# Optimization experiments

Measured on AMD Instinct MI355X. Metric: run time of the kernel, lower is better.

## Reference

```python
import jax, jax.numpy as jnp
import numpy as np

PAD = 4  # matches init pad


def setup_inputs() -> dict:
    key = jax.random.key(0)
    k1, k2 = jax.random.split(key)
    n, t, c, h, w = 256, 4, 3, 96, 96
    # raw pixel values in [0, 255) like uint8 frames, stored as float32
    img = jax.random.uniform(k1, (n, t, c, h, w), dtype=jnp.float32) * 255.0
    # integer shift per batch element, same across time: randint(0, 2*pad+1, (n, 2))
    shift = jax.random.randint(k2, (n, 2), 0, 2 * PAD + 1, dtype=jnp.int32)
    return {"img": img, "shift": shift}


def reference(img, shift):
    """ShiftImgPreprocessor.forward (train path, eval=False).

    Original: normalize, replicate-pad by PAD, then bilinear grid_sample with a
    grid of pixel-center coords offset by an integer shift (in units of
    2/(h+2*pad)). Because the shift is an exact integer number of pixels and the
    base grid hits pixel centers exactly (align_corners=False), the bilinear
    sample is an exact integer gather: out[b,t,c,i,j] = padded[b,t,c,i+sy, j+sx].
    All sampled coords stay inside the padded image, so padding_mode='zeros'
    never triggers.
    """
    n, t, c, h, w = img.shape
    x = img / 255.0 - 0.5
    # replicate pad H and W by PAD
    xp = jnp.pad(x, ((0, 0), (0, 0), (0, 0), (PAD, PAD), (PAD, PAD)), mode="edge")

    def shift_one(xp_b, s):
        # s[0] is the x (width) shift, s[1] is the y (height) shift
        return jax.lax.dynamic_slice(xp_b, (0, 0, s[1], s[0]), (t, c, h, w))

    return jax.vmap(shift_one)(xp, shift)
```

## Files before the change

### kernel.cpp

```cpp
#include <hip/hip_runtime.h>


#define PAD 4
#define NB  256
#define TT  4
#define CC  3
#define HH  96
#define WW  96
#define W4  (WW / 4)
#define ROWS_PER_B (TT * CC * HH)
#define V4_PER_B (ROWS_PER_B * W4)
#define BLOCK 256

typedef float vfloat4 __attribute__((ext_vector_type(4)));

__global__ __launch_bounds__(BLOCK) void ShiftImgPreprocessor_36679020708143_kernel(
    const float* __restrict__ img,
    const int*   __restrict__ shift,
    float*       __restrict__ out)
{
    const int b = blockIdx.y;
    const int v = blockIdx.x * BLOCK + threadIdx.x;

    const int j4 = v % W4;
    const int r_ = v / W4;
    const int i  = r_ % HH;
    const int tc = r_ / HH;

    const int dx = shift[2 * b + 0] - PAD;
    const int dy = shift[2 * b + 1] - PAD;

    const int yy = min(max(i + dy, 0), HH - 1);

    const size_t plane = ((size_t)b * (TT * CC) + tc) * (size_t)(HH * WW);
    const float* __restrict__ srcrow = img + plane + (size_t)yy * WW;

    const int j = j4 * 4;
    const float k = 1.0f / 255.0f;
    vfloat4 o;

    if (j4 == 0 || j4 == W4 - 1) {
        const int x0 = min(max(j + 0 + dx, 0), WW - 1);
        const int x1 = min(max(j + 1 + dx, 0), WW - 1);
        const int x2 = min(max(j + 2 + dx, 0), WW - 1);
        const int x3 = min(max(j + 3 + dx, 0), WW - 1);
        o = (vfloat4){srcrow[x0], srcrow[x1], srcrow[x2], srcrow[x3]};
    } else {
        const int s  = j + dx;
        const int a4 = s >> 2;
        const int r  = dx & 3;
        const vfloat4* __restrict__ sv = (const vfloat4*)srcrow;
        const vfloat4 V0 = sv[a4];
        const vfloat4 V1 = sv[min(a4 + 1, W4 - 1)];
        switch (r) {
            case 0:  o = V0; break;
            case 1:  o = (vfloat4){V0.y, V0.z, V0.w, V1.x}; break;
            case 2:  o = (vfloat4){V0.z, V0.w, V1.x, V1.y}; break;
            default: o = (vfloat4){V0.w, V1.x, V1.y, V1.z}; break;
        }
    }

    o = o * k - 0.5f;

    vfloat4* outv = (vfloat4*)(out + plane + (size_t)i * WW + j);
    *outv = o;
}

extern "C" void kernel_launch(void* const* d_in, const int* in_sizes, int n_in,
                              void* d_out, int out_size, void* d_ws, size_t ws_size,
                              hipStream_t stream) {
    const float* img   = (const float*)d_in[0];
    const int*   shift = (const int*)d_in[1];
    float*       out   = (float*)d_out;

    dim3 grid(V4_PER_B / BLOCK, NB);
    ShiftImgPreprocessor_36679020708143_kernel<<<grid, BLOCK, 0, stream>>>(img, shift, out);
}
```

Measured before the change: 194.0 us.

## Use persistent grid-stride blocks with software-pipelined load of next tile

```diff
diff --git a/kernel.cpp b/kernel.cpp
--- a/kernel.cpp
+++ b/kernel.cpp
@@ -8,62 +8,99 @@
 #define HH  96
 #define WW  96
 #define W4  (WW / 4)
-#define ROWS_PER_B (TT * CC * HH)
-#define V4_PER_B (ROWS_PER_B * W4)
+#define TC  (TT * CC)
+#define HW  (HH * WW)
+#define V4B (TC * HH * W4)
 #define BLOCK 256
+#define TPB (V4B / BLOCK)
+#define TILES (NB * TPB)
+#define NBLK 2048
 
 typedef float vfloat4 __attribute__((ext_vector_type(4)));
 
-__global__ __launch_bounds__(BLOCK) void ShiftImgPreprocessor_36679020708143_kernel(
+__device__ __forceinline__ void stage_load(
+    int tile, int tid,
+    const float* __restrict__ img, const int* __restrict__ shift,
+    float* __restrict__ out,
+    vfloat4* A, vfloat4* B, int* s_, int* dx_, float** dst)
+{
+    const int b    = tile / TPB;
+    const int tloc = tile - b * TPB;
+    const int vb   = tloc * BLOCK + tid;
+    const int j4   = vb % W4;
+    const int r_   = vb / W4;
+    const int i    = r_ % HH;
+    const int tc   = r_ / HH;
+
+    const int dx = shift[2 * b + 0] - PAD;
+    const int dy = shift[2 * b + 1] - PAD;
+    const int yy = min(max(i + dy, 0), HH - 1);
+
+    const size_t plane = ((size_t)b * TC + tc) * HW;
+    const vfloat4* __restrict__ sv = (const vfloat4*)(img + plane + (size_t)yy * WW);
+
+    const int j  = j4 * 4;
+    const int s  = j + dx;
+    const int a4 = s >> 2;
+    const int a0 = min(max(a4, 0), W4 - 1);
+    const int a1 = min(a4 + 1, W4 - 1);
+
+    *A = sv[a0];
+    *B = sv[a1];
+    *s_  = s;
+    *dx_ = dx;
+    *dst = out + plane + (size_t)i * WW + j;
+}
+
+__device__ __forceinline__ void consume_store(
+    vfloat4 A, vfloat4 B, int s, int dx, float* __restrict__ dst)
+{
+    vfloat4 o;
+    switch (dx & 3) {
+        case 0:  o = A; break;
+        case 1:  o = (vfloat4){A.y, A.z, A.w, B.x}; break;
+        case 2:  o = (vfloat4){A.z, A.w, B.x, B.y}; break;
+        default: o = (vfloat4){A.w, B.x, B.y, B.z}; break;
+    }
+    if (s < 0 || s > WW - 4) {
+        switch (dx) {
+            case -4: o = (vfloat4){A.x, A.x, A.x, A.x}; break;
+            case -3: o = (vfloat4){A.x, A.x, A.x, A.x}; break;
+            case -2: o = (vfloat4){A.x, A.x, A.x, A.y}; break;
+            case -1: o = (vfloat4){A.x, A.x, A.y, A.z}; break;
+            case  1: o = (vfloat4){A.y, A.z, A.w, A.w}; break;
+            case  2: o = (vfloat4){A.z, A.w, A.w, A.w}; break;
+            default: o = (vfloat4){A.w, A.w, A.w, A.w}; break;
+        }
+    }
+    o = o * (1.0f / 255.0f) - 0.5f;
+    *(vfloat4*)dst = o;
+}
+
+__global__ __launch_bounds__(BLOCK, 8) void ShiftImgPreprocessor_36679020708143_kernel(
     const float* __restrict__ img,
     const int*   __restrict__ shift,
     float*       __restrict__ out)
 {
-    const int b = blockIdx.y;
-    const int v = blockIdx.x * BLOCK + threadIdx.x;
+    const int tid = threadIdx.x;
+    int tile = blockIdx.x;
 
-    const int j4 = v % W4;
-    const int r_ = v / W4;
-    const int i  = r_ % HH;
-    const int tc = r_ / HH;
+    vfloat4 A0, B0; int s0, dx0; float* d0;
+    stage_load(tile, tid, img, shift, out, &A0, &B0, &s0, &dx0, &d0);
 
-    const int dx = shift[2 * b + 0] - PAD;
-    const int dy = shift[2 * b + 1] - PAD;
-
-    const int yy = min(max(i + dy, 0), HH - 1);
-
-    const size_t plane = ((size_t)b * (TT * CC) + tc) * (size_t)(HH * WW);
-    const float* __restrict__ srcrow = img + plane + (size_t)yy * WW;
-
-    const int j = j4 * 4;
-    const float k = 1.0f / 255.0f;
-    vfloat4 o;
-
-    if (j4 == 0 || j4 == W4 - 1) {
-        const int x0 = min(max(j + 0 + dx, 0), WW - 1);
-        const int x1 = min(max(j + 1 + dx, 0), WW - 1);
-        const int x2 = min(max(j + 2 + dx, 0), WW - 1);
-        const int x3 = min(max(j + 3 + dx, 0), WW - 1);
-        o = (vfloat4){srcrow[x0], srcrow[x1], srcrow[x2], srcrow[x3]};
-    } else {
-        const int s  = j + dx;
-        const int a4 = s >> 2;
-        const int r  = dx & 3;
-        const vfloat4* __restrict__ sv = (const vfloat4*)srcrow;
-        const vfloat4 V0 = sv[a4];
-        const vfloat4 V1 = sv[min(a4 + 1, W4 - 1)];
-        switch (r) {
-            case 0:  o = V0; break;
-            case 1:  o = (vfloat4){V0.y, V0.z, V0.w, V1.x}; break;
-            case 2:  o = (vfloat4){V0.z, V0.w, V1.x, V1.y}; break;
-            default: o = (vfloat4){V0.w, V1.x, V1.y, V1.z}; break;
+    for (;;) {
+        const int nt = tile + NBLK;
+        if (nt < TILES) {
+            vfloat4 A1, B1; int s1, dx1; float* d1;
+            stage_load(nt, tid, img, shift, out, &A1, &B1, &s1, &dx1, &d1);
+            consume_store(A0, B0, s0, dx0, d0);
+            A0 = A1; B0 = B1; s0 = s1; dx0 = dx1; d0 = d1;
+            tile = nt;
+        } else {
+            consume_store(A0, B0, s0, dx0, d0);
+            break;
         }
     }
-
-    o = o * k - 0.5f;
-
-    vfloat4* outv = (vfloat4*)(out + plane + (size_t)i * WW + j);
-    *outv = o;
 }
 
 extern "C" void kernel_launch(void* const* d_in, const int* in_sizes, int n_in,
@@ -73,6 +110,5 @@
     const int*   shift = (const int*)d_in[1];
     float*       out   = (float*)d_out;
 
-    dim3 grid(V4_PER_B / BLOCK, NB);
-    ShiftImgPreprocessor_36679020708143_kernel<<<grid, BLOCK, 0, stream>>>(img, shift, out);
+    ShiftImgPreprocessor_36679020708143_kernel<<<dim3(NBLK), BLOCK, 0, stream>>>(img, shift, out);
 }
```

After: 198.2 us. 1.02x slower.

## Stage row tiles in LDS with replicated halo for shifted copy

Applied to the files above, without the earlier changes.

```diff
diff --git a/kernel.cpp b/kernel.cpp
--- a/kernel.cpp
+++ b/kernel.cpp
@@ -8,9 +8,15 @@
 #define HH  96
 #define WW  96
 #define W4  (WW / 4)
-#define ROWS_PER_B (TT * CC * HH)
-#define V4_PER_B (ROWS_PER_B * W4)
-#define BLOCK 256
+#define TC  (TT * CC)
+#define HW  (HH * WW)
+#define RPB 16
+#define BPP (HH / RPB)
+#define BLOCK 128
+#define F4PB (RPB * W4)
+#define PERT (F4PB / BLOCK)
+#define LROW 104
+#define NBLK (NB * TC * BPP)
 
 typedef float vfloat4 __attribute__((ext_vector_type(4)));
 
@@ -19,51 +25,55 @@
     const int*   __restrict__ shift,
     float*       __restrict__ out)
 {
-    const int b = blockIdx.y;
-    const int v = blockIdx.x * BLOCK + threadIdx.x;
+    __shared__ float lds[RPB][LROW];
 
-    const int j4 = v % W4;
-    const int r_ = v / W4;
-    const int i  = r_ % HH;
-    const int tc = r_ / HH;
+    const int blk = blockIdx.x;
+    const int bp  = blk / BPP;
+    const int rb  = blk - bp * BPP;
+    const int b   = bp / TC;
+    const int i0  = rb * RPB;
+    const int t   = threadIdx.x;
 
     const int dx = shift[2 * b + 0] - PAD;
     const int dy = shift[2 * b + 1] - PAD;
 
-    const int yy = min(max(i + dy, 0), HH - 1);
+    const size_t plane = (size_t)bp * HW;
+    const float* __restrict__ src = img + plane;
+    float*       __restrict__ dst = out + plane;
 
-    const size_t plane = ((size_t)b * (TT * CC) + tc) * (size_t)(HH * WW);
-    const float* __restrict__ srcrow = img + plane + (size_t)yy * WW;
+    #pragma unroll
+    for (int p = 0; p < PERT; ++p) {
+        const int u = t + p * BLOCK;
+        const int k = u / W4;
+        const int c = u - k * W4;
+        const int yy = min(max(i0 + k + dy, 0), HH - 1);
+        const vfloat4 v = *(const vfloat4*)(src + (size_t)yy * WW + 4 * c);
+        *(vfloat4*)&lds[k][4 + 4 * c] = v;
+    }
+    __syncthreads();
 
-    const int j = j4 * 4;
-    const float k = 1.0f / 255.0f;
-    vfloat4 o;
+    if (t < RPB) {
+        const float e = lds[t][4];
+        lds[t][0] = e; lds[t][1] = e; lds[t][2] = e; lds[t][3] = e;
+    } else if (t < 2 * RPB) {
+        const int k = t - RPB;
+        const float e = lds[k][99];
+        lds[k][100] = e; lds[k][101] = e; lds[k][102] = e; lds[k][103] = e;
+    }
+    __syncthreads();
 
-    if (j4 == 0 || j4 == W4 - 1) {
-        const int x0 = min(max(j + 0 + dx, 0), WW - 1);
-        const int x1 = min(max(j + 1 + dx, 0), WW - 1);
-        const int x2 = min(max(j + 2 + dx, 0), WW - 1);
-        const int x3 = min(max(j + 3 + dx, 0), WW - 1);
-        o = (vfloat4){srcrow[x0], srcrow[x1], srcrow[x2], srcrow[x3]};
-    } else {
-        const int s  = j + dx;
-        const int a4 = s >> 2;
-        const int r  = dx & 3;
-        const vfloat4* __restrict__ sv = (const vfloat4*)srcrow;
-        const vfloat4 V0 = sv[a4];
-        const vfloat4 V1 = sv[min(a4 + 1, W4 - 1)];
-        switch (r) {
-            case 0:  o = V0; break;
-            case 1:  o = (vfloat4){V0.y, V0.z, V0.w, V1.x}; break;
-            case 2:  o = (vfloat4){V0.z, V0.w, V1.x, V1.y}; break;
-            default: o = (vfloat4){V0.w, V1.x, V1.y, V1.z}; break;
-        }
+    const float kk = 1.0f / 255.0f;
+    #pragma unroll
+    for (int p = 0; p < PERT; ++p) {
+        const int u = t + p * BLOCK;
+        const int k = u / W4;
+        const int c = u - k * W4;
+        const float* lp = &lds[k][0] + (4 + 4 * c + dx);
+        vfloat4 v;
+        __builtin_memcpy(&v, lp, sizeof(v));
+        v = v * kk - 0.5f;
+        *(vfloat4*)(dst + (size_t)(i0 + k) * WW + 4 * c) = v;
     }
-
-    o = o * k - 0.5f;
-
-    vfloat4* outv = (vfloat4*)(out + plane + (size_t)i * WW + j);
-    *outv = o;
 }
 
 extern "C" void kernel_launch(void* const* d_in, const int* in_sizes, int n_in,
@@ -73,6 +83,5 @@
     const int*   shift = (const int*)d_in[1];
     float*       out   = (float*)d_out;
 
-    dim3 grid(V4_PER_B / BLOCK, NB);
-    ShiftImgPreprocessor_36679020708143_kernel<<<grid, BLOCK, 0, stream>>>(img, shift, out);
+    ShiftImgPreprocessor_36679020708143_kernel<<<dim3(NBLK), BLOCK, 0, stream>>>(img, shift, out);
 }
```

Measured after the change: 197.9 us. 2.0% more time.

## Process half-planes per block with software-pipelined multi-load register staging

Applied to the files above, without the earlier changes.

```diff
diff --git a/kernel.cpp b/kernel.cpp
--- a/kernel.cpp
+++ b/kernel.cpp
@@ -8,9 +8,11 @@
 #define HH  96
 #define WW  96
 #define W4  (WW / 4)
-#define ROWS_PER_B (TT * CC * HH)
-#define V4_PER_B (ROWS_PER_B * W4)
-#define BLOCK 256
+#define TC  (TT * CC)
+#define HW  (HH * WW)
+#define BLOCK 128
+#define NHP (NB * TC * 2)
+#define STAGES 9
 
 typedef float vfloat4 __attribute__((ext_vector_type(4)));
 
@@ -19,51 +21,69 @@
     const int*   __restrict__ shift,
     float*       __restrict__ out)
 {
-    const int b = blockIdx.y;
-    const int v = blockIdx.x * BLOCK + threadIdx.x;
-
-    const int j4 = v % W4;
-    const int r_ = v / W4;
-    const int i  = r_ % HH;
-    const int tc = r_ / HH;
+    const int bid = blockIdx.x;
+    const int hp = (bid & 7) * (NHP / 8) + (bid >> 3);
+    const int pl = hp >> 1;
+    const int h  = hp & 1;
+    const int b  = pl / TC;
+    const int t  = threadIdx.x;
 
     const int dx = shift[2 * b + 0] - PAD;
     const int dy = shift[2 * b + 1] - PAD;
 
-    const int yy = min(max(i + dy, 0), HH - 1);
+    const float* __restrict__ src = img + (size_t)pl * HW;
+    float*       __restrict__ dst = out + (size_t)pl * HW;
 
-    const size_t plane = ((size_t)b * (TT * CC) + tc) * (size_t)(HH * WW);
-    const float* __restrict__ srcrow = img + plane + (size_t)yy * WW;
+    vfloat4 A[STAGES], B[STAGES];
 
-    const int j = j4 * 4;
-    const float k = 1.0f / 255.0f;
-    vfloat4 o;
+    #define PRE(i) { \
+        const int u  = (i) * BLOCK + t;                \
+        const int k  = h * 48 + u / W4;                \
+        const int c  = u % W4;                         \
+        const int yy = min(max(k + dy, 0), HH - 1); \
+        const vfloat4* __restrict__ sv = (const vfloat4*)(src + yy * WW); \
+        const int s  = 4 * c + dx;                     \
+        const int a4 = s >> 2; \
+        const int a0 = min(max(a4, 0), W4 - 1); \
+        const int a1 = min(a4 + 1, W4 - 1); \
+        A[i] = sv[a0]; \
+        B[i] = sv[a1]; }
 
-    if (j4 == 0 || j4 == W4 - 1) {
-        const int x0 = min(max(j + 0 + dx, 0), WW - 1);
-        const int x1 = min(max(j + 1 + dx, 0), WW - 1);
-        const int x2 = min(max(j + 2 + dx, 0), WW - 1);
-        const int x3 = min(max(j + 3 + dx, 0), WW - 1);
-        o = (vfloat4){srcrow[x0], srcrow[x1], srcrow[x2], srcrow[x3]};
-    } else {
-        const int s  = j + dx;
-        const int a4 = s >> 2;
-        const int r  = dx & 3;
-        const vfloat4* __restrict__ sv = (const vfloat4*)srcrow;
-        const vfloat4 V0 = sv[a4];
-        const vfloat4 V1 = sv[min(a4 + 1, W4 - 1)];
-        switch (r) {
-            case 0:  o = V0; break;
-            case 1:  o = (vfloat4){V0.y, V0.z, V0.w, V1.x}; break;
-            case 2:  o = (vfloat4){V0.z, V0.w, V1.x, V1.y}; break;
-            default: o = (vfloat4){V0.w, V1.x, V1.y, V1.z}; break;
-        }
-    }
+    #define CON(i) { \
+        const int u = (i) * BLOCK + t; \
+        const int k = h * 48 + u / W4; \
+        const int c = u % W4; \
+        const int s = 4 * c + dx; \
+        const vfloat4 Av = A[i], Bv = B[i]; \
+        vfloat4 o; \
+        switch (dx & 3) {                               \
+            case 0:  o = Av; break; \
+            case 1:  o = (vfloat4){Av.y, Av.z, Av.w, Bv.x}; break; \
+            case 2:  o = (vfloat4){Av.z, Av.w, Bv.x, Bv.y}; break; \
+            default: o = (vfloat4){Av.w, Bv.x, Bv.y, Bv.z}; break; } \
+        if (s < 0 || s > WW - 4) {                      \
+            switch (dx) {                               \
+                case -4: \
+                case -3: o = (vfloat4){Av.x, Av.x, Av.x, Av.x}; break; \
+                case -2: o = (vfloat4){Av.x, Av.x, Av.x, Av.y}; break; \
+                case -1: o = (vfloat4){Av.x, Av.x, Av.y, Av.z}; break; \
+                case  1: o = (vfloat4){Av.y, Av.z, Av.w, Av.w}; break; \
+                case  2: o = (vfloat4){Av.z, Av.w, Av.w, Av.w}; break; \
+                default: o = (vfloat4){Av.w, Av.w, Av.w, Av.w}; break; } } \
+        o = o * (1.0f / 255.0f) - 0.5f; \
+        *(vfloat4*)(dst + (size_t)k * WW + 4 * c) = o; }
 
-    o = o * k - 0.5f;
+    PRE(0) PRE(1) PRE(2)
+    CON(0) PRE(3)
+    CON(1) PRE(4)
+    CON(2) PRE(5)
+    CON(3) PRE(6)
+    CON(4) PRE(7)
+    CON(5) PRE(8)
+    CON(6) CON(7) CON(8)
 
-    vfloat4* outv = (vfloat4*)(out + plane + (size_t)i * WW + j);
-    *outv = o;
+    #undef PRE
+    #undef CON
 }
 
 extern "C" void kernel_launch(void* const* d_in, const int* in_sizes, int n_in,
@@ -73,6 +93,5 @@
     const int*   shift = (const int*)d_in[1];
     float*       out   = (float*)d_out;
 
-    dim3 grid(V4_PER_B / BLOCK, NB);
-    ShiftImgPreprocessor_36679020708143_kernel<<<grid, BLOCK, 0, stream>>>(img, shift, out);
+    ShiftImgPreprocessor_36679020708143_kernel<<<dim3(NHP), BLOCK, 0, stream>>>(img, shift, out);
 }
```

Result: slower. 200.5 us (+3.4%).
